# Kernel optimization log

Hardware: AMD Instinct MI355X
Metric: run time of the kernel (lower is better)

Reference implementation:

```python
import jax, jax.numpy as jnp
import numpy as np

B, S, D = 1, 2048, 2048
HQ, HKV, HD = 32, 8, 64
EXPAND = HQ // HKV

def _rotate_half(x):
    x1, x2 = x[..., : x.shape[-1] // 2], x[..., x.shape[-1] // 2 :]
    return jnp.concatenate((-x2, x1), axis=-1)

def setup_inputs() -> dict:
    key = jax.random.key(0)
    k1, k2, k3 = jax.random.split(key, 3)
    hidden_states = jax.random.normal(k1, (B, S, D), dtype=jnp.float32)
    # Llama weight init scale ~ small
    Wq = jax.random.normal(k2, (HQ * HD, D), dtype=jnp.float32) * 0.02
    Wk = jax.random.normal(k3, (HKV * HD, D), dtype=jnp.float32) * 0.02
    # true rotary cos/sin tables, shape [B, S, HD]
    inv_freq = 1.0 / (10000.0 ** (jnp.arange(0, HD, 2, dtype=jnp.float32) / HD))
    pos = jnp.arange(S, dtype=jnp.float32)
    freqs = pos[:, None] * inv_freq[None, :]            # [S, HD/2]
    emb = jnp.concatenate((freqs, freqs), axis=-1)       # [S, HD]
    cos = jnp.broadcast_to(jnp.cos(emb)[None], (B, S, HD))
    sin = jnp.broadcast_to(jnp.sin(emb)[None], (B, S, HD))
    attn_mask = jnp.zeros((B, 1, S, S), dtype=jnp.float32)  # accepted but unused by the module
    return {"hidden_states": hidden_states, "cos": cos, "sin": sin,
            "attn_mask": attn_mask, "Wq": Wq, "Wk": Wk}

def reference(hidden_states, cos, sin, attn_mask, Wq, Wk):
    b, s, _ = hidden_states.shape
    # projections (nn.Linear, no bias): x @ W.T
    q = hidden_states @ Wq.T                              # [b, s, HQ*HD]
    k = hidden_states @ Wk.T                              # [b, s, HKV*HD]
    q = q.reshape(b, s, HQ, HD).transpose(0, 2, 1, 3)     # [b, HQ, s, HD]
    k = k.reshape(b, s, HKV, HD).transpose(0, 2, 1, 3)    # [b, HKV, s, HD]
    c = cos[:, None, :, :]                                # unsqueeze_dim=1
    sn = sin[:, None, :, :]
    q = q * c + _rotate_half(q) * sn
    k = k * c + _rotate_half(k) * sn
    k = jnp.repeat(k, EXPAND, axis=1)                     # GQA repeat_interleave -> [b, HQ, s, HD]
    scores = jnp.einsum('bhqd,bhkd->bhqk', q, k)          # NO 1/sqrt(d) scaling (faithful)
    return jax.nn.softmax(scores, axis=-1)
```

## Files before the change

### kernel.cpp

```cpp
#include <hip/hip_runtime.h>
#include <hip/hip_bf16.h>

typedef _Float16 half8 __attribute__((ext_vector_type(8)));
typedef float floatx4 __attribute__((ext_vector_type(4)));

#define SEQ 2048
#define DIM 2048
#define HQ 32
#define HKV 8
#define HD 64
#define NQ (HQ*HD)
#define NK (HKV*HD)
#define NTOT (NQ+NK)

#define GLOAD_LDS16(g, l) \
    __builtin_amdgcn_global_load_lds( \
        (const __attribute__((address_space(1))) void*)(g), \
        (__attribute__((address_space(3))) void*)(l), 16, 0, 0)

__global__ __launch_bounds__(256) void convert_kernel(
    const float* __restrict__ X, const float* __restrict__ Wq,
    const float* __restrict__ Wk, _Float16* __restrict__ Xh,
    _Float16* __restrict__ Wh)
{
    const long c   = (long)blockIdx.x * 256 + threadIdx.x;
    const long nxc = (long)SEQ * DIM / 8;
    const float* src;
    _Float16* dst;
    if (c < nxc) {
        src = X + c * 8;
        dst = Xh + c * 8;
    } else {
        long f = (c - nxc) * 8;
        src = (f < (long)NQ * DIM) ? Wq + f : Wk + (f - (long)NQ * DIM);
        dst = Wh + f;
    }
    float4 a = ((const float4*)src)[0];
    float4 b = ((const float4*)src)[1];
    half8 h = {(_Float16)a.x, (_Float16)a.y, (_Float16)a.z, (_Float16)a.w,
               (_Float16)b.x, (_Float16)b.y, (_Float16)b.z, (_Float16)b.w};
    *(half8*)dst = h;
}

__global__ __launch_bounds__(256) void gemm1_kernel(
    const _Float16* __restrict__ Xh, const _Float16* __restrict__ Wh,
    const float* __restrict__ cosb, const float* __restrict__ sinb,
    _Float16* __restrict__ qout, _Float16* __restrict__ kout)
{
    __shared__ __align__(16) _Float16 lsA[64 * 64];
    __shared__ __align__(16) _Float16 lsB[128 * 64];
    const int tid  = threadIdx.x;
    const int lane = tid & 63;
    const int wv   = tid >> 6;
    const int wm   = wv & 1, wn = wv >> 1;
    const int m    = lane & 15, quad = lane >> 4;
    const int s0   = blockIdx.x * 64;
    const int n0   = blockIdx.y * 128;

    floatx4 acc[2][4];
    #pragma unroll
    for (int i = 0; i < 2; i++)
        #pragma unroll
        for (int j = 0; j < 4; j++)
            acc[i][j] = floatx4{0.f, 0.f, 0.f, 0.f};

    for (int k0 = 0; k0 < DIM; k0 += 64) {
        __syncthreads();
        #pragma unroll
        for (int r = 0; r < 2; r++) {
            int c    = r * 256 + tid;
            int row  = c >> 3;
            int chg  = (c & 7) ^ (row & 7);
            GLOAD_LDS16(Xh + (long)(s0 + row) * DIM + k0 + chg * 8,
                        (char*)lsA + (r * 256 + wv * 64) * 16);
        }
        #pragma unroll
        for (int r = 0; r < 4; r++) {
            int c    = r * 256 + tid;
            int row  = c >> 3;
            int chg  = (c & 7) ^ (row & 7);
            GLOAD_LDS16(Wh + (long)(n0 + row) * DIM + k0 + chg * 8,
                        (char*)lsB + (r * 256 + wv * 64) * 16);
        }
        __syncthreads();

        #pragma unroll
        for (int kk = 0; kk < 2; kk++) {
            half8 aF[2], bF[4];
            #pragma unroll
            for (int i = 0; i < 2; i++) {
                int row = wm * 32 + i * 16 + m;
                int pc  = ((kk << 2) | quad) ^ (m & 7);
                aF[i] = *(const half8*)(lsA + row * 64 + pc * 8);
            }
            #pragma unroll
            for (int j = 0; j < 4; j++) {
                int row = wn * 64 + j * 16 + m;
                int pc  = ((kk << 2) | quad) ^ (m & 7);
                bF[j] = *(const half8*)(lsB + row * 64 + pc * 8);
            }
            #pragma unroll
            for (int i = 0; i < 2; i++)
                #pragma unroll
                for (int j = 0; j < 4; j++)
                    acc[i][j] = __builtin_amdgcn_mfma_f32_16x16x32_f16(
                        aF[i], bF[j], acc[i][j], 0, 0, 0);
        }
    }

    #pragma unroll
    for (int i = 0; i < 2; i++) {
        #pragma unroll
        for (int reg = 0; reg < 4; reg++) {
            int s = s0 + wm * 32 + i * 16 + quad * 4 + reg;
            #pragma unroll
            for (int j = 0; j < 4; j++) {
                int col = n0 + wn * 64 + j * 16 + m;
                int d   = j * 16 + m;
                float v = acc[i][j][reg];
                float partner = (j < 2) ? -acc[i][j + 2][reg] : acc[i][j - 2][reg];
                float cs = cosb[s * HD + d];
                float sn = sinb[s * HD + d];
                _Float16 o = (_Float16)(v * cs + partner * sn);
                if (col < NQ) {
                    int hq = col >> 6;
                    qout[((long)hq * SEQ + s) * HD + d] = o;
                } else {
                    int hk = (col - NQ) >> 6;
                    kout[((long)hk * SEQ + s) * HD + d] = o;
                }
            }
        }
    }
}

__global__ __launch_bounds__(512) void attn_kernel(
    const _Float16* __restrict__ qf, const _Float16* __restrict__ kf,
    float* __restrict__ out)
{
    __shared__ float redm[8][16];
    __shared__ float redl[8][16];
    const int tid  = threadIdx.x;
    const int lane = tid & 63;
    const int w    = tid >> 6;
    const int m    = lane & 15, quad = lane >> 4;
    const int qb   = blockIdx.x;
    const int h    = blockIdx.y;
    const int kvh  = h >> 2;
    const int s0   = qb * 16;

    const _Float16* qbase = qf + ((long)h * SEQ + s0) * HD;
    const _Float16* kbase = kf + (long)kvh * SEQ * HD;

    half8 bQ0 = *(const half8*)(qbase + (long)m * HD + quad * 8);
    half8 bQ1 = *(const half8*)(qbase + (long)m * HD + 32 + quad * 8);

    floatx4 acc[16];
    #pragma unroll
    for (int ct = 0; ct < 16; ct++) {
        int n0 = w * 256 + ct * 16;
        const _Float16* kp = kbase + (long)(n0 + m) * HD + quad * 8;
        half8 aK0 = *(const half8*)(kp);
        half8 aK1 = *(const half8*)(kp + 32);
        floatx4 a = floatx4{0.f, 0.f, 0.f, 0.f};
        a = __builtin_amdgcn_mfma_f32_16x16x32_f16(aK0, bQ0, a, 0, 0, 0);
        a = __builtin_amdgcn_mfma_f32_16x16x32_f16(aK1, bQ1, a, 0, 0, 0);
        acc[ct] = a;
    }

    float lm = acc[0][0];
    #pragma unroll
    for (int ct = 0; ct < 16; ct++)
        #pragma unroll
        for (int r = 0; r < 4; r++) lm = fmaxf(lm, acc[ct][r]);
    lm = fmaxf(lm, __shfl_xor(lm, 16));
    lm = fmaxf(lm, __shfl_xor(lm, 32));
    if (quad == 0) redm[w][m] = lm;
    __syncthreads();
    float g = redm[0][m];
    #pragma unroll
    for (int ww = 1; ww < 8; ww++) g = fmaxf(g, redm[ww][m]);

    float ls = 0.f;
    #pragma unroll
    for (int ct = 0; ct < 16; ct++) {
        #pragma unroll
        for (int r = 0; r < 4; r++) {
            float e = __expf(acc[ct][r] - g);
            acc[ct][r] = e;
            ls += e;
        }
    }
    ls += __shfl_xor(ls, 16);
    ls += __shfl_xor(ls, 32);
    if (quad == 0) redl[w][m] = ls;
    __syncthreads();
    float tot = 0.f;
    #pragma unroll
    for (int ww = 0; ww < 8; ww++) tot += redl[ww][m];
    float inv = 1.0f / tot;

    float* obase = out + ((long)h * SEQ + s0 + m) * SEQ + w * 256 + quad * 4;
    #pragma unroll
    for (int ct = 0; ct < 16; ct++) {
        floatx4 v = acc[ct];
        v[0] *= inv; v[1] *= inv; v[2] *= inv; v[3] *= inv;
        *(floatx4*)(obase + ct * 16) = v;
    }
}

extern "C" void kernel_launch(void* const* d_in, const int* in_sizes, int n_in,
                              void* d_out, int out_size, void* d_ws, size_t ws_size,
                              hipStream_t stream) {
    const float* hidden = (const float*)d_in[0];
    const float* cosb   = (const float*)d_in[1];
    const float* sinb   = (const float*)d_in[2];
    const float* Wq     = (const float*)d_in[4];
    const float* Wk     = (const float*)d_in[5];
    float* out = (float*)d_out;

    char* ws = (char*)d_ws;
    _Float16* Xh = (_Float16*)ws;
    _Float16* Wh = (_Float16*)(ws + 8388608);
    _Float16* qf = (_Float16*)(ws + 8388608 + 10485760);
    _Float16* kf = (_Float16*)(ws + 8388608 + 10485760 + 8388608);

    convert_kernel<<<4608, 256, 0, stream>>>(hidden, Wq, Wk, Xh, Wh);
    gemm1_kernel<<<dim3(32, 20), 256, 0, stream>>>(Xh, Wh, cosb, sinb, qf, kf);
    attn_kernel<<<dim3(128, 32), 512, 0, stream>>>(qf, kf, out);
}
```

Measured before the change: 686.3 us.

## Enlarge GEMM tile to 128x128, prefetch K fragments, fold log2e into Q

The projection GEMM tile grows from 64x128 to 128x128, so each wave computes 4x4 MFMA tiles and the grid halves, raising data reuse per LDS load. The attention kernel now software-prefetches the next K fragment while the current MFMAs run. Q is pre-scaled by log2(e) in the epilogue so softmax can use exp2f instead of __expf. The larger tile uses more registers and LDS, which may lower occupancy, and the 320-block grid underfills a 256-CU device for a second wave.

```diff
diff --git a/kernel.cpp b/kernel.cpp
--- a/kernel.cpp
+++ b/kernel.cpp
@@ -12,6 +12,7 @@
 #define NQ (HQ*HD)
 #define NK (HKV*HD)
 #define NTOT (NQ+NK)
+#define LOG2E 1.44269504088896340736f
 
 #define GLOAD_LDS16(g, l) \
     __builtin_amdgcn_global_load_lds( \
@@ -47,19 +48,19 @@
     const float* __restrict__ cosb, const float* __restrict__ sinb,
     _Float16* __restrict__ qout, _Float16* __restrict__ kout)
 {
-    __shared__ __align__(16) _Float16 lsA[64 * 64];
+    __shared__ __align__(16) _Float16 lsA[128 * 64];
     __shared__ __align__(16) _Float16 lsB[128 * 64];
     const int tid  = threadIdx.x;
     const int lane = tid & 63;
     const int wv   = tid >> 6;
     const int wm   = wv & 1, wn = wv >> 1;
     const int m    = lane & 15, quad = lane >> 4;
-    const int s0   = blockIdx.x * 64;
+    const int s0   = blockIdx.x * 128;
     const int n0   = blockIdx.y * 128;
 
-    floatx4 acc[2][4];
-    #pragma unroll
-    for (int i = 0; i < 2; i++)
+    floatx4 acc[4][4];
+    #pragma unroll
+    for (int i = 0; i < 4; i++)
         #pragma unroll
         for (int j = 0; j < 4; j++)
             acc[i][j] = floatx4{0.f, 0.f, 0.f, 0.f};
@@ -67,7 +68,7 @@
     for (int k0 = 0; k0 < DIM; k0 += 64) {
         __syncthreads();
         #pragma unroll
-        for (int r = 0; r < 2; r++) {
+        for (int r = 0; r < 4; r++) {
             int c    = r * 256 + tid;
             int row  = c >> 3;
             int chg  = (c & 7) ^ (row & 7);
@@ -86,21 +87,16 @@
 
         #pragma unroll
         for (int kk = 0; kk < 2; kk++) {
-            half8 aF[2], bF[4];
-            #pragma unroll
-            for (int i = 0; i < 2; i++) {
-                int row = wm * 32 + i * 16 + m;
-                int pc  = ((kk << 2) | quad) ^ (m & 7);
-                aF[i] = *(const half8*)(lsA + row * 64 + pc * 8);
-            }
-            #pragma unroll
-            for (int j = 0; j < 4; j++) {
-                int row = wn * 64 + j * 16 + m;
-                int pc  = ((kk << 2) | quad) ^ (m & 7);
-                bF[j] = *(const half8*)(lsB + row * 64 + pc * 8);
-            }
-            #pragma unroll
-            for (int i = 0; i < 2; i++)
+            half8 aF[4], bF[4];
+            const int pc = ((kk << 2) | quad) ^ (m & 7);
+            #pragma unroll
+            for (int i = 0; i < 4; i++)
+                aF[i] = *(const half8*)(lsA + (wm * 64 + i * 16 + m) * 64 + pc * 8);
+            #pragma unroll
+            for (int j = 0; j < 4; j++)
+                bF[j] = *(const half8*)(lsB + (wn * 64 + j * 16 + m) * 64 + pc * 8);
+            #pragma unroll
+            for (int i = 0; i < 4; i++)
                 #pragma unroll
                 for (int j = 0; j < 4; j++)
                     acc[i][j] = __builtin_amdgcn_mfma_f32_16x16x32_f16(
@@ -109,10 +105,10 @@
     }
 
     #pragma unroll
-    for (int i = 0; i < 2; i++) {
+    for (int i = 0; i < 4; i++) {
         #pragma unroll
         for (int reg = 0; reg < 4; reg++) {
-            int s = s0 + wm * 32 + i * 16 + quad * 4 + reg;
+            int s = s0 + wm * 64 + i * 16 + quad * 4 + reg;
             #pragma unroll
             for (int j = 0; j < 4; j++) {
                 int col = n0 + wn * 64 + j * 16 + m;
@@ -121,13 +117,13 @@
                 float partner = (j < 2) ? -acc[i][j + 2][reg] : acc[i][j - 2][reg];
                 float cs = cosb[s * HD + d];
                 float sn = sinb[s * HD + d];
-                _Float16 o = (_Float16)(v * cs + partner * sn);
+                float o  = v * cs + partner * sn;
                 if (col < NQ) {
                     int hq = col >> 6;
-                    qout[((long)hq * SEQ + s) * HD + d] = o;
+                    qout[((long)hq * SEQ + s) * HD + d] = (_Float16)(o * LOG2E);
                 } else {
                     int hk = (col - NQ) >> 6;
-                    kout[((long)hk * SEQ + s) * HD + d] = o;
+                    kout[((long)hk * SEQ + s) * HD + d] = (_Float16)o;
                 }
             }
         }
@@ -156,16 +152,23 @@
     half8 bQ1 = *(const half8*)(qbase + (long)m * HD + 32 + quad * 8);
 
     floatx4 acc[16];
+    const _Float16* kp = kbase + (long)(w * 256 + m) * HD + quad * 8;
+    half8 aK0 = *(const half8*)(kp);
+    half8 aK1 = *(const half8*)(kp + 32);
     #pragma unroll
     for (int ct = 0; ct < 16; ct++) {
-        int n0 = w * 256 + ct * 16;
-        const _Float16* kp = kbase + (long)(n0 + m) * HD + quad * 8;
-        half8 aK0 = *(const half8*)(kp);
-        half8 aK1 = *(const half8*)(kp + 32);
+        half8 nK0, nK1;
+        if (ct < 15) {
+            const _Float16* np = kbase + (long)(w * 256 + (ct + 1) * 16 + m) * HD + quad * 8;
+            nK0 = *(const half8*)(np);
+            nK1 = *(const half8*)(np + 32);
+        }
         floatx4 a = floatx4{0.f, 0.f, 0.f, 0.f};
         a = __builtin_amdgcn_mfma_f32_16x16x32_f16(aK0, bQ0, a, 0, 0, 0);
         a = __builtin_amdgcn_mfma_f32_16x16x32_f16(aK1, bQ1, a, 0, 0, 0);
         acc[ct] = a;
+        aK0 = nK0;
+        aK1 = nK1;
     }
 
     float lm = acc[0][0];
@@ -186,7 +189,7 @@
     for (int ct = 0; ct < 16; ct++) {
         #pragma unroll
         for (int r = 0; r < 4; r++) {
-            float e = __expf(acc[ct][r] - g);
+            float e = exp2f(acc[ct][r] - g);
             acc[ct][r] = e;
             ls += e;
         }
@@ -226,6 +229,6 @@
     _Float16* kf = (_Float16*)(ws + 8388608 + 10485760 + 8388608);
 
     convert_kernel<<<4608, 256, 0, stream>>>(hidden, Wq, Wk, Xh, Wh);
-    gemm1_kernel<<<dim3(32, 20), 256, 0, stream>>>(Xh, Wh, cosb, sinb, qf, kf);
+    gemm1_kernel<<<dim3(16, 20), 256, 0, stream>>>(Xh, Wh, cosb, sinb, qf, kf);
     attn_kernel<<<dim3(128, 32), 512, 0, stream>>>(qf, kf, out);
 }
```

After: 702.3 us. +2.3%, slower.
